# Optimization experiments

Measured on AMD Instinct MI355X. Metric: run time of the kernel, lower is better.

The kernel has to match this reference:

```python
import jax, jax.numpy as jnp
import numpy as np

NUM_EXPERTS = 8

def setup_inputs() -> dict:
    key = jax.random.key(0)
    k1, k2, k3, k4, k5 = jax.random.split(key, 5)
    T, D, H, O, E, K = 4096, 1024, 2048, 1024, NUM_EXPERTS, 2
    hidden_states = jax.random.normal(k1, (T, D), dtype=jnp.float32)
    top_k_indices = jax.random.randint(k2, (T, K), 0, E, dtype=jnp.int64)
    top_k_weights = jax.random.uniform(k3, (T, K), dtype=jnp.float32)
    gate_up_proj = jax.random.normal(k4, (E, 2 * H, D), dtype=jnp.float32) * 0.02
    down_proj = jax.random.normal(k5, (E, O, H), dtype=jnp.float32) * 0.02
    return {
        "hidden_states": hidden_states,
        "top_k_indices": top_k_indices,
        "top_k_weights": top_k_weights,
        "gate_up_proj": gate_up_proj,
        "down_proj": down_proj,
    }


def _moe(hidden_states, top_k_weights, gate_up_proj, down_proj, top_k_indices):
    # Mathematically identical to the torch per-token-gather loop, expressed as
    # dense all-expert compute + sparse combine (non-selected experts get weight 0).
    T = hidden_states.shape[0]
    E = gate_up_proj.shape[0]
    # [T, E, 2H]
    gate_up = jnp.einsum('td,ehd->teh', hidden_states, gate_up_proj)
    gate, up = jnp.split(gate_up, 2, axis=-1)
    h = jax.nn.silu(gate) * up  # [T, E, H]
    expert_out = jnp.einsum('teh,eoh->teo', h, down_proj)  # [T, E, O]
    # combine weights: scatter top-k routing weights into [T, E]
    combine = jnp.zeros((T, E), dtype=hidden_states.dtype)
    rows = jnp.arange(T)[:, None]
    combine = combine.at[rows, top_k_indices].add(top_k_weights)
    return jnp.einsum('teo,te->to', expert_out, combine)


def reference(hidden_states, top_k_indices, top_k_weights, gate_up_proj, down_proj):
    return _moe(hidden_states, top_k_weights, gate_up_proj, down_proj, top_k_indices)
```

## Files before the change

### kernel.cpp

```cpp
#include <hip/hip_runtime.h>
#include <stdint.h>

#define TOKS 4096
#define DIM  1024
#define HID  2048
#define OUTD 1024
#define NE   8
#define MP   9216
#define NBR  72

typedef __bf16 bf16;
typedef bf16 bf16x8 __attribute__((ext_vector_type(8)));
typedef float f32x4 __attribute__((ext_vector_type(4)));
typedef __attribute__((address_space(1))) void gvoid;
typedef __attribute__((address_space(3))) void lvoid;

#define WGU_OFF  0ull
#define WD_OFF   (WGU_OFF + 67108864ull)
#define XG_OFF   (WD_OFF  + 33554432ull)
#define H_OFF    (XG_OFF  + 18874368ull)
#define TK_OFF   (H_OFF   + 37748736ull)
#define META_OFF (TK_OFF  + 36864ull)
#define T2S_OFF  (META_OFF + 1024ull)
#define O0_OFF   WGU_OFF
#define O1_OFF   (WGU_OFF + 18874368ull)

__device__ __forceinline__ unsigned short f2bf(float f) {
  union { float f; unsigned u; } v; v.f = f;
  unsigned r = (v.u + 0x7FFFu + ((v.u >> 16) & 1u)) >> 16;
  return (unsigned short)r;
}
__device__ __forceinline__ float bf2f(unsigned short h) {
  union { unsigned u; float f; } v; v.u = ((unsigned)h) << 16; return v.f;
}
__device__ __forceinline__ unsigned pack2(float a, float b) {
  return (unsigned)f2bf(a) | ((unsigned)f2bf(b) << 16);
}
__device__ __forceinline__ void cp16(const void* g, void* l) {
  __builtin_amdgcn_global_load_lds((gvoid*)(void*)g, (lvoid*)l, 16, 0, 0);
}

#define CONVB_GU (NE * 2 * HID * DIM / 4 / 1024)
#define CONVB_X  (TOKS * DIM / 4 / 1024)
__global__ __launch_bounds__(1024) void route_conv_kernel(
    const int* __restrict__ idx, int* __restrict__ table,
    int* __restrict__ slot_token, int* __restrict__ tok2slot,
    const float4* __restrict__ srcGu, uint2* __restrict__ dstGu,
    const float4* __restrict__ srcX, uint2* __restrict__ dstXg) {
  if (blockIdx.x != 0) {
    int b = (int)blockIdx.x - 1;
    const float4* src; uint2* dst; int i;
    if (b < CONVB_GU) { i = b * 1024 + threadIdx.x; src = srcGu; dst = dstGu; }
    else              { i = (b - CONVB_GU) * 1024 + threadIdx.x; src = srcX; dst = dstXg; }
    float4 v = src[i];
    uint2 o; o.x = pack2(v.x, v.y); o.y = pack2(v.z, v.w);
    dst[i] = o;
    return;
  }
  __shared__ int cnt[NE], offs[NE], cur[NE];
  const int tid = threadIdx.x, lane = tid & 63;
  for (int i = tid; i < MP; i += 1024) slot_token[i] = -1;
  if (tid < NE) cnt[tid] = 0;
  __syncthreads();
  int myE[8];
#pragma unroll
  for (int c = 0; c < 8; ++c) myE[c] = idx[c * 1024 + tid];
#pragma unroll
  for (int c = 0; c < 8; ++c) {
    int e = myE[c];
#pragma unroll
    for (int ex = 0; ex < NE; ++ex) {
      unsigned long long m = __ballot(e == ex);
      if (lane == 0 && m) atomicAdd(&cnt[ex], __popcll(m));
    }
  }
  __syncthreads();
  if (tid == 0) {
    int cum = 0;
    for (int e = 0; e < NE; ++e) {
      offs[e] = cum; cur[e] = 0;
      int nb = (cnt[e] + 127) >> 7;
      int bb = cum >> 7;
      for (int b = 0; b < nb; ++b) table[bb + b] = e;
      cum += nb << 7;
    }
    for (int b = cum >> 7; b < NBR; ++b) table[b] = -1;
  }
  __syncthreads();
#pragma unroll
  for (int c = 0; c < 8; ++c) {
    int e = myE[c];
    int pos = 0;
#pragma unroll
    for (int ex = 0; ex < NE; ++ex) {
      unsigned long long m = __ballot(e == ex);
      if (e == ex) {
        int rank = __popcll(m & ((1ull << lane) - 1ull));
        int leader = __ffsll(m) - 1;
        int base = 0;
        if (lane == leader) base = atomicAdd(&cur[ex], __popcll(m));
        base = __shfl(base, leader);
        pos = offs[ex] + base + rank;
      }
    }
    slot_token[pos] = (c * 1024 + tid) >> 1;
    tok2slot[c * 1024 + tid] = pos;
  }
}

__global__ void combine_kernel(const unsigned short* __restrict__ O0,
                               const unsigned short* __restrict__ O1,
                               const int* __restrict__ tok2slot,
                               const float* __restrict__ wts, float4* __restrict__ out) {
  int t = blockIdx.x, c = threadIdx.x;
  int s0 = tok2slot[2 * t], s1 = tok2slot[2 * t + 1];
  float w0 = wts[2 * t], w1 = wts[2 * t + 1];
  uint2 a0 = ((const uint2*)(O0 + (size_t)s0 * OUTD))[c];
  uint2 b0 = ((const uint2*)(O1 + (size_t)s0 * OUTD))[c];
  uint2 a1 = ((const uint2*)(O0 + (size_t)s1 * OUTD))[c];
  uint2 b1 = ((const uint2*)(O1 + (size_t)s1 * OUTD))[c];
  float4 o;
  o.x = w0 * (bf2f(a0.x & 0xFFFF) + bf2f(b0.x & 0xFFFF)) + w1 * (bf2f(a1.x & 0xFFFF) + bf2f(b1.x & 0xFFFF));
  o.y = w0 * (bf2f(a0.x >> 16)    + bf2f(b0.x >> 16))    + w1 * (bf2f(a1.x >> 16)    + bf2f(b1.x >> 16));
  o.z = w0 * (bf2f(a0.y & 0xFFFF) + bf2f(b0.y & 0xFFFF)) + w1 * (bf2f(a1.y & 0xFFFF) + bf2f(b1.y & 0xFFFF));
  o.w = w0 * (bf2f(a0.y >> 16)    + bf2f(b0.y >> 16))    + w1 * (bf2f(a1.y >> 16)    + bf2f(b1.y >> 16));
  out[(size_t)t * (OUTD / 4) + c] = o;
}

#define WD_N4 (NE * OUTD * HID / 4)
#define CVT_NB 576
__global__ __launch_bounds__(256) void gemm1_kernel(
    const unsigned short* __restrict__ Xg,
    const unsigned short* __restrict__ Wgu,
    unsigned short* __restrict__ Hbuf,
    const int* __restrict__ table,
    const int* __restrict__ slot_token,
    const float4* __restrict__ srcD, uint2* __restrict__ dstD) {
  if (blockIdx.x >= 32) {
    const int cid = (blockIdx.x - 32) + 8 * blockIdx.y;
    const int NT = CVT_NB * 256;
    for (int i = cid * 256 + (int)threadIdx.x; i < WD_N4; i += NT) {
      float4 v = srcD[i];
      uint2 o; o.x = pack2(v.x, v.y); o.y = pack2(v.z, v.w);
      dstD[i] = o;
    }
    return;
  }
  int e = table[blockIdx.y];
  if (e < 0) return;
  const int tid = threadIdx.x;
  const int lane = tid & 63, wave = tid >> 6;
  const int wm = wave >> 1, wn = wave & 1;
  const int lr = lane & 15, quad = lane >> 4;

  __shared__ bf16 As[128 * 64];
  __shared__ bf16 Bg[64 * 64];
  __shared__ bf16 Bu[64 * 64];

  const int r0 = tid >> 3;
  size_t abase[4];
#pragma unroll
  for (int i = 0; i < 4; ++i) {
    int t = slot_token[blockIdx.y * 128 + i * 32 + r0];
    if (t < 0) t = 0;
    abase[i] = (size_t)t * DIM;
  }

  const unsigned short* Wg_base = Wgu + (size_t)e * 2 * HID * DIM + (size_t)(blockIdx.x * 64) * DIM;
  const unsigned short* Wu_base = Wg_base + (size_t)HID * DIM;

  f32x4 accg[4][2] = {}; f32x4 accu[4][2] = {};

  for (int kt = 0; kt < DIM / 64; ++kt) {
    const int kb = kt * 64;
#pragma unroll
    for (int i = 0; i < 4; ++i) {
      int s = i * 256 + tid, row = s >> 3, pc = s & 7, gc = pc ^ (row & 7);
      cp16(Xg + abase[i] + kb + gc * 8, (void*)(As + row * 64 + pc * 8));
    }
#pragma unroll
    for (int i = 0; i < 2; ++i) {
      int s = i * 256 + tid, row = s >> 3, pc = s & 7, gc = pc ^ (row & 7);
      cp16(Wg_base + (size_t)row * DIM + kb + gc * 8, (void*)(Bg + row * 64 + pc * 8));
      cp16(Wu_base + (size_t)row * DIM + kb + gc * 8, (void*)(Bu + row * 64 + pc * 8));
    }
    __syncthreads();
#pragma unroll
    for (int ks = 0; ks < 2; ++ks) {
      bf16x8 a[4], bg[2], bu[2];
#pragma unroll
      for (int i = 0; i < 4; ++i) {
        int row = wm * 64 + i * 16 + lr;
        int pc = (ks * 4 + quad) ^ (row & 7);
        a[i] = *(const bf16x8*)(As + row * 64 + pc * 8);
      }
#pragma unroll
      for (int j = 0; j < 2; ++j) {
        int row = wn * 32 + j * 16 + lr;
        int pc = (ks * 4 + quad) ^ (row & 7);
        bg[j] = *(const bf16x8*)(Bg + row * 64 + pc * 8);
        bu[j] = *(const bf16x8*)(Bu + row * 64 + pc * 8);
      }
#pragma unroll
      for (int i = 0; i < 4; ++i)
#pragma unroll
        for (int j = 0; j < 2; ++j) {
          accg[i][j] = __builtin_amdgcn_mfma_f32_16x16x32_bf16(a[i], bg[j], accg[i][j], 0, 0, 0);
          accu[i][j] = __builtin_amdgcn_mfma_f32_16x16x32_bf16(a[i], bu[j], accu[i][j], 0, 0, 0);
        }
    }
    __syncthreads();
  }

  const int rowBase = blockIdx.y * 128 + wm * 64;
  const int colBase = blockIdx.x * 64 + wn * 32;
#pragma unroll
  for (int i = 0; i < 4; ++i)
#pragma unroll
    for (int r = 0; r < 4; ++r) {
      int row = rowBase + i * 16 + quad * 4 + r;
#pragma unroll
      for (int j = 0; j < 2; ++j) {
        float g = accg[i][j][r], u = accu[i][j][r];
        float s = g / (1.0f + __expf(-g));
        Hbuf[(size_t)row * HID + colBase + j * 16 + lr] = f2bf(s * u);
      }
    }
}

__global__ __launch_bounds__(256) void gemm2_kernel(
    const unsigned short* __restrict__ Hbuf,
    const unsigned short* __restrict__ Wd,
    unsigned short* __restrict__ O0,
    unsigned short* __restrict__ O1,
    const int* __restrict__ table) {
  int e = table[blockIdx.y];
  if (e < 0) return;
  const int tid = threadIdx.x;
  const int lane = tid & 63, wave = tid >> 6;
  const int wm = wave >> 1, wn = wave & 1;
  const int lr = lane & 15, quad = lane >> 4;
  const int kslice = blockIdx.z;

  __shared__ bf16 As[128 * 64];
  __shared__ bf16 Bs[128 * 64];

  const unsigned short* A_base = Hbuf + (size_t)blockIdx.y * 128 * HID + kslice * (HID / 2);
  const unsigned short* B_base = Wd + (size_t)e * OUTD * HID + (size_t)(blockIdx.x * 128) * HID
                               + kslice * (HID / 2);

  f32x4 acc[4][4] = {};

  for (int kt = 0; kt < (HID / 2) / 64; ++kt) {
    const int kb = kt * 64;
#pragma unroll
    for (int i = 0; i < 4; ++i) {
      int s = i * 256 + tid, row = s >> 3, pc = s & 7, gc = pc ^ (row & 7);
      cp16(A_base + (size_t)row * HID + kb + gc * 8, (void*)(As + row * 64 + pc * 8));
      cp16(B_base + (size_t)row * HID + kb + gc * 8, (void*)(Bs + row * 64 + pc * 8));
    }
    __syncthreads();
#pragma unroll
    for (int ks = 0; ks < 2; ++ks) {
      bf16x8 a[4], b[4];
#pragma unroll
      for (int i = 0; i < 4; ++i) {
        int row = wm * 64 + i * 16 + lr;
        int pc = (ks * 4 + quad) ^ (row & 7);
        a[i] = *(const bf16x8*)(As + row * 64 + pc * 8);
      }
#pragma unroll
      for (int j = 0; j < 4; ++j) {
        int row = wn * 64 + j * 16 + lr;
        int pc = (ks * 4 + quad) ^ (row & 7);
        b[j] = *(const bf16x8*)(Bs + row * 64 + pc * 8);
      }
#pragma unroll
      for (int i = 0; i < 4; ++i)
#pragma unroll
        for (int j = 0; j < 4; ++j)
          acc[i][j] = __builtin_amdgcn_mfma_f32_16x16x32_bf16(a[i], b[j], acc[i][j], 0, 0, 0);
    }
    __syncthreads();
  }

  unsigned short* O = kslice ? O1 : O0;
  const int rowBase = blockIdx.y * 128 + wm * 64;
  const int colBase = blockIdx.x * 128 + wn * 64;
#pragma unroll
  for (int i = 0; i < 4; ++i)
#pragma unroll
    for (int r = 0; r < 4; ++r) {
      int row = rowBase + i * 16 + quad * 4 + r;
      unsigned short* Orow = O + (size_t)row * OUTD + colBase;
#pragma unroll
      for (int j = 0; j < 4; ++j)
        Orow[j * 16 + lr] = f2bf(acc[i][j][r]);
    }
}

extern "C" void kernel_launch(void* const* d_in, const int* in_sizes, int n_in,
                              void* d_out, int out_size, void* d_ws, size_t ws_size,
                              hipStream_t stream) {
  const float* X     = (const float*)d_in[0];
  const int*   idx   = (const int*)d_in[1];
  const float* wts   = (const float*)d_in[2];
  const float* WguF  = (const float*)d_in[3];
  const float* WdF   = (const float*)d_in[4];
  float* out = (float*)d_out;

  char* base = (char*)d_ws;
  unsigned short* Wgu = (unsigned short*)(base + WGU_OFF);
  unsigned short* Wd  = (unsigned short*)(base + WD_OFF);
  unsigned short* Xg  = (unsigned short*)(base + XG_OFF);
  unsigned short* Hb  = (unsigned short*)(base + H_OFF);
  unsigned short* O0  = (unsigned short*)(base + O0_OFF);
  unsigned short* O1  = (unsigned short*)(base + O1_OFF);
  int* slot_token = (int*)(base + TK_OFF);
  int* table      = (int*)(base + META_OFF);
  int* tok2slot   = (int*)(base + T2S_OFF);

  route_conv_kernel<<<1 + CONVB_GU + CONVB_X, 1024, 0, stream>>>(idx, table, slot_token, tok2slot,
      (const float4*)WguF, (uint2*)Wgu, (const float4*)X, (uint2*)Xg);
  gemm1_kernel<<<dim3(40, NBR), 256, 0, stream>>>(Xg, Wgu, Hb, table, slot_token,
      (const float4*)WdF, (uint2*)Wd);
  gemm2_kernel<<<dim3(OUTD / 128, NBR, 2), 256, 0, stream>>>(Hb, Wd, O0, O1, table);
  combine_kernel<<<TOKS, 256, 0, stream>>>(O0, O1, tok2slot, wts, (float4*)out);
}
```

Measured before the change: 398.6 us.

## Grid-stride weight conversion, split gemm1 launch, remap gemm2 blocks for L2 locality

The fp32-to-bf16 conversion now uses a fixed grid of 2560 blocks with a grid-stride loop, replacing one block per 1024 float4s. gemm1 is issued as two launches over halves of the row blocks, passing a ybase offset. gemm2 remaps its linear block id so that blocks which run at the same time share experts and weight tiles, aiming to improve L2 reuse across the XCD-interleaved dispatch. These changes add index arithmetic and one extra launch in exchange for better cache locality and less block-scheduling overhead.

```diff
diff --git a/kernel.cpp b/kernel.cpp
--- a/kernel.cpp
+++ b/kernel.cpp
@@ -40,8 +40,10 @@
   __builtin_amdgcn_global_load_lds((gvoid*)(void*)g, (lvoid*)l, 16, 0, 0);
 }
 
-#define CONVB_GU (NE * 2 * HID * DIM / 4 / 1024)
-#define CONVB_X  (TOKS * DIM / 4 / 1024)
+#define N4_GU (NE * 2 * HID * DIM / 4)
+#define N4_X  (TOKS * DIM / 4)
+#define N4_TOT (N4_GU + N4_X)
+#define NCONV 2560
 __global__ __launch_bounds__(1024) void route_conv_kernel(
     const int* __restrict__ idx, int* __restrict__ table,
     int* __restrict__ slot_token, int* __restrict__ tok2slot,
@@ -49,12 +51,13 @@
     const float4* __restrict__ srcX, uint2* __restrict__ dstXg) {
   if (blockIdx.x != 0) {
     int b = (int)blockIdx.x - 1;
-    const float4* src; uint2* dst; int i;
-    if (b < CONVB_GU) { i = b * 1024 + threadIdx.x; src = srcGu; dst = dstGu; }
-    else              { i = (b - CONVB_GU) * 1024 + threadIdx.x; src = srcX; dst = dstXg; }
-    float4 v = src[i];
-    uint2 o; o.x = pack2(v.x, v.y); o.y = pack2(v.z, v.w);
-    dst[i] = o;
+    for (int i = b * 1024 + (int)threadIdx.x; i < N4_TOT; i += NCONV * 1024) {
+      float4 v; uint2* dp;
+      if (i < N4_GU) { v = srcGu[i]; dp = dstGu + i; }
+      else           { v = srcX[i - N4_GU]; dp = dstXg + (i - N4_GU); }
+      uint2 o; o.x = pack2(v.x, v.y); o.y = pack2(v.z, v.w);
+      *dp = o;
+    }
     return;
   }
   __shared__ int cnt[NE], offs[NE], cur[NE];
@@ -135,9 +138,11 @@
     unsigned short* __restrict__ Hbuf,
     const int* __restrict__ table,
     const int* __restrict__ slot_token,
-    const float4* __restrict__ srcD, uint2* __restrict__ dstD) {
+    const float4* __restrict__ srcD, uint2* __restrict__ dstD,
+    int ybase) {
+  const int by = ybase + (int)blockIdx.y;
   if (blockIdx.x >= 32) {
-    const int cid = (blockIdx.x - 32) + 8 * blockIdx.y;
+    const int cid = ((int)blockIdx.x - 32) + 8 * by;
     const int NT = CVT_NB * 256;
     for (int i = cid * 256 + (int)threadIdx.x; i < WD_N4; i += NT) {
       float4 v = srcD[i];
@@ -146,7 +151,7 @@
     }
     return;
   }
-  int e = table[blockIdx.y];
+  int e = table[by];
   if (e < 0) return;
   const int tid = threadIdx.x;
   const int lane = tid & 63, wave = tid >> 6;
@@ -161,7 +166,7 @@
   size_t abase[4];
 #pragma unroll
   for (int i = 0; i < 4; ++i) {
-    int t = slot_token[blockIdx.y * 128 + i * 32 + r0];
+    int t = slot_token[by * 128 + i * 32 + r0];
     if (t < 0) t = 0;
     abase[i] = (size_t)t * DIM;
   }
@@ -212,7 +217,7 @@
     __syncthreads();
   }
 
-  const int rowBase = blockIdx.y * 128 + wm * 64;
+  const int rowBase = by * 128 + wm * 64;
   const int colBase = blockIdx.x * 64 + wn * 32;
 #pragma unroll
   for (int i = 0; i < 4; ++i)
@@ -234,19 +239,25 @@
     unsigned short* __restrict__ O0,
     unsigned short* __restrict__ O1,
     const int* __restrict__ table) {
-  int e = table[blockIdx.y];
+  const int h = (int)blockIdx.x + 8 * (int)blockIdx.y + 576 * (int)blockIdx.z;
+  const int c = h & 7, j = h >> 3;
+  const int wx = j & 7;
+  const int gi = c * 18 + (j >> 3);
+  const int wy = gi % 72, wz = gi / 72;
+
+  int e = table[wy];
   if (e < 0) return;
   const int tid = threadIdx.x;
   const int lane = tid & 63, wave = tid >> 6;
   const int wm = wave >> 1, wn = wave & 1;
   const int lr = lane & 15, quad = lane >> 4;
-  const int kslice = blockIdx.z;
+  const int kslice = wz;
 
   __shared__ bf16 As[128 * 64];
   __shared__ bf16 Bs[128 * 64];
 
-  const unsigned short* A_base = Hbuf + (size_t)blockIdx.y * 128 * HID + kslice * (HID / 2);
-  const unsigned short* B_base = Wd + (size_t)e * OUTD * HID + (size_t)(blockIdx.x * 128) * HID
+  const unsigned short* A_base = Hbuf + (size_t)wy * 128 * HID + kslice * (HID / 2);
+  const unsigned short* B_base = Wd + (size_t)e * OUTD * HID + (size_t)(wx * 128) * HID
                                + kslice * (HID / 2);
 
   f32x4 acc[4][4] = {};
@@ -270,23 +281,23 @@
         a[i] = *(const bf16x8*)(As + row * 64 + pc * 8);
       }
 #pragma unroll
-      for (int j = 0; j < 4; ++j) {
-        int row = wn * 64 + j * 16 + lr;
+      for (int j2 = 0; j2 < 4; ++j2) {
+        int row = wn * 64 + j2 * 16 + lr;
         int pc = (ks * 4 + quad) ^ (row & 7);
-        b[j] = *(const bf16x8*)(Bs + row * 64 + pc * 8);
+        b[j2] = *(const bf16x8*)(Bs + row * 64 + pc * 8);
       }
 #pragma unroll
       for (int i = 0; i < 4; ++i)
 #pragma unroll
-        for (int j = 0; j < 4; ++j)
-          acc[i][j] = __builtin_amdgcn_mfma_f32_16x16x32_bf16(a[i], b[j], acc[i][j], 0, 0, 0);
+        for (int j2 = 0; j2 < 4; ++j2)
+          acc[i][j2] = __builtin_amdgcn_mfma_f32_16x16x32_bf16(a[i], b[j2], acc[i][j2], 0, 0, 0);
     }
     __syncthreads();
   }
 
   unsigned short* O = kslice ? O1 : O0;
-  const int rowBase = blockIdx.y * 128 + wm * 64;
-  const int colBase = blockIdx.x * 128 + wn * 64;
+  const int rowBase = wy * 128 + wm * 64;
+  const int colBase = wx * 128 + wn * 64;
 #pragma unroll
   for (int i = 0; i < 4; ++i)
 #pragma unroll
@@ -294,8 +305,8 @@
       int row = rowBase + i * 16 + quad * 4 + r;
       unsigned short* Orow = O + (size_t)row * OUTD + colBase;
 #pragma unroll
-      for (int j = 0; j < 4; ++j)
-        Orow[j * 16 + lr] = f2bf(acc[i][j][r]);
+      for (int j2 = 0; j2 < 4; ++j2)
+        Orow[j2 * 16 + lr] = f2bf(acc[i][j2][r]);
     }
 }
 
@@ -320,10 +331,12 @@
   int* table      = (int*)(base + META_OFF);
   int* tok2slot   = (int*)(base + T2S_OFF);
 
-  route_conv_kernel<<<1 + CONVB_GU + CONVB_X, 1024, 0, stream>>>(idx, table, slot_token, tok2slot,
+  route_conv_kernel<<<1 + NCONV, 1024, 0, stream>>>(idx, table, slot_token, tok2slot,
       (const float4*)WguF, (uint2*)Wgu, (const float4*)X, (uint2*)Xg);
-  gemm1_kernel<<<dim3(40, NBR), 256, 0, stream>>>(Xg, Wgu, Hb, table, slot_token,
-      (const float4*)WdF, (uint2*)Wd);
-  gemm2_kernel<<<dim3(OUTD / 128, NBR, 2), 256, 0, stream>>>(Hb, Wd, O0, O1, table);
+  gemm1_kernel<<<dim3(40, 36), 256, 0, stream>>>(Xg, Wgu, Hb, table, slot_token,
+      (const float4*)WdF, (uint2*)Wd, 0);
+  gemm1_kernel<<<dim3(40, 36), 256, 0, stream>>>(Xg, Wgu, Hb, table, slot_token,
+      (const float4*)WdF, (uint2*)Wd, 36);
+  gemm2_kernel<<<dim3(8, NBR, 2), 256, 0, stream>>>(Hb, Wd, O0, O1, table);
   combine_kernel<<<TOKS, 256, 0, stream>>>(O0, O1, tok2slot, wts, (float4*)out);
 }
```

Measured after the change: 405.3 us. No clear change (+1.7%).

## Double-buffer LDS tiles with K=32 stages in both expert GEMMs

Applied to the files above, without the earlier changes.

Both grouped GEMM kernels now split K into 32-wide stages held in two LDS buffers. The async copy of the next stage is issued before the MFMAs on the current stage, so global loads overlap with compute instead of sitting behind a barrier. The swizzle is adapted to 32-element rows. Each stage does half as many MFMAs per barrier, and total LDS per block is unchanged.

```diff
diff --git a/kernel.cpp b/kernel.cpp
--- a/kernel.cpp
+++ b/kernel.cpp
@@ -137,7 +137,7 @@
     const int* __restrict__ slot_token,
     const float4* __restrict__ srcD, uint2* __restrict__ dstD) {
   if (blockIdx.x >= 32) {
-    const int cid = (blockIdx.x - 32) + 8 * blockIdx.y;
+    const int cid = ((int)blockIdx.x - 32) + 8 * (int)blockIdx.y;
     const int NT = CVT_NB * 256;
     for (int i = cid * 256 + (int)threadIdx.x; i < WD_N4; i += NT) {
       float4 v = srcD[i];
@@ -153,15 +153,15 @@
   const int wm = wave >> 1, wn = wave & 1;
   const int lr = lane & 15, quad = lane >> 4;
 
-  __shared__ bf16 As[128 * 64];
-  __shared__ bf16 Bg[64 * 64];
-  __shared__ bf16 Bu[64 * 64];
-
-  const int r0 = tid >> 3;
-  size_t abase[4];
-#pragma unroll
-  for (int i = 0; i < 4; ++i) {
-    int t = slot_token[blockIdx.y * 128 + i * 32 + r0];
+  __shared__ bf16 As[2][128 * 32];
+  __shared__ bf16 Bg[2][64 * 32];
+  __shared__ bf16 Bu[2][64 * 32];
+
+  const int r0 = tid >> 2;
+  size_t abase[2];
+#pragma unroll
+  for (int i = 0; i < 2; ++i) {
+    int t = slot_token[blockIdx.y * 128 + i * 64 + r0];
     if (t < 0) t = 0;
     abase[i] = (size_t)t * DIM;
   }
@@ -171,44 +171,53 @@
 
   f32x4 accg[4][2] = {}; f32x4 accu[4][2] = {};
 
-  for (int kt = 0; kt < DIM / 64; ++kt) {
-    const int kb = kt * 64;
+  auto stage = [&](bf16* as, bf16* bg, bf16* bu, int kt) {
+    const int kb = kt * 32;
+#pragma unroll
+    for (int i = 0; i < 2; ++i) {
+      int s = i * 256 + tid, row = s >> 2, p = s & 3, gc = p ^ ((row >> 1) & 3);
+      cp16(Xg + abase[i] + kb + gc * 8, (void*)(as + row * 32 + p * 8));
+    }
+    {
+      int s = tid, row = s >> 2, p = s & 3, gc = p ^ ((row >> 1) & 3);
+      cp16(Wg_base + (size_t)row * DIM + kb + gc * 8, (void*)(bg + row * 32 + p * 8));
+      cp16(Wu_base + (size_t)row * DIM + kb + gc * 8, (void*)(bu + row * 32 + p * 8));
+    }
+  };
+
+  auto compute = [&](const bf16* as, const bf16* bg, const bf16* bu) {
+    bf16x8 a[4], g[2], u[2];
 #pragma unroll
     for (int i = 0; i < 4; ++i) {
-      int s = i * 256 + tid, row = s >> 3, pc = s & 7, gc = pc ^ (row & 7);
-      cp16(Xg + abase[i] + kb + gc * 8, (void*)(As + row * 64 + pc * 8));
-    }
-#pragma unroll
-    for (int i = 0; i < 2; ++i) {
-      int s = i * 256 + tid, row = s >> 3, pc = s & 7, gc = pc ^ (row & 7);
-      cp16(Wg_base + (size_t)row * DIM + kb + gc * 8, (void*)(Bg + row * 64 + pc * 8));
-      cp16(Wu_base + (size_t)row * DIM + kb + gc * 8, (void*)(Bu + row * 64 + pc * 8));
-    }
+      int row = wm * 64 + i * 16 + lr;
+      int p = quad ^ ((row >> 1) & 3);
+      a[i] = *(const bf16x8*)(as + row * 32 + p * 8);
+    }
+#pragma unroll
+    for (int j = 0; j < 2; ++j) {
+      int row = wn * 32 + j * 16 + lr;
+      int p = quad ^ ((row >> 1) & 3);
+      g[j] = *(const bf16x8*)(bg + row * 32 + p * 8);
+      u[j] = *(const bf16x8*)(bu + row * 32 + p * 8);
+    }
+#pragma unroll
+    for (int i = 0; i < 4; ++i)
+#pragma unroll
+      for (int j = 0; j < 2; ++j) {
+        accg[i][j] = __builtin_amdgcn_mfma_f32_16x16x32_bf16(a[i], g[j], accg[i][j], 0, 0, 0);
+        accu[i][j] = __builtin_amdgcn_mfma_f32_16x16x32_bf16(a[i], u[j], accu[i][j], 0, 0, 0);
+      }
+  };
+
+  stage(As[0], Bg[0], Bu[0], 0);
+  __syncthreads();
+#pragma unroll 1
+  for (int kt = 0; kt < DIM / 32; kt += 2) {
+    stage(As[1], Bg[1], Bu[1], kt + 1);
+    compute(As[0], Bg[0], Bu[0]);
     __syncthreads();
-#pragma unroll
-    for (int ks = 0; ks < 2; ++ks) {
-      bf16x8 a[4], bg[2], bu[2];
-#pragma unroll
-      for (int i = 0; i < 4; ++i) {
-        int row = wm * 64 + i * 16 + lr;
-        int pc = (ks * 4 + quad) ^ (row & 7);
-        a[i] = *(const bf16x8*)(As + row * 64 + pc * 8);
-      }
-#pragma unroll
-      for (int j = 0; j < 2; ++j) {
-        int row = wn * 32 + j * 16 + lr;
-        int pc = (ks * 4 + quad) ^ (row & 7);
-        bg[j] = *(const bf16x8*)(Bg + row * 64 + pc * 8);
-        bu[j] = *(const bf16x8*)(Bu + row * 64 + pc * 8);
-      }
-#pragma unroll
-      for (int i = 0; i < 4; ++i)
-#pragma unroll
-        for (int j = 0; j < 2; ++j) {
-          accg[i][j] = __builtin_amdgcn_mfma_f32_16x16x32_bf16(a[i], bg[j], accg[i][j], 0, 0, 0);
-          accu[i][j] = __builtin_amdgcn_mfma_f32_16x16x32_bf16(a[i], bu[j], accu[i][j], 0, 0, 0);
-        }
-    }
+    if (kt + 2 < DIM / 32) stage(As[0], Bg[0], Bu[0], kt + 2);
+    compute(As[1], Bg[1], Bu[1]);
     __syncthreads();
   }
 
@@ -242,8 +251,8 @@
   const int lr = lane & 15, quad = lane >> 4;
   const int kslice = blockIdx.z;
 
-  __shared__ bf16 As[128 * 64];
-  __shared__ bf16 Bs[128 * 64];
+  __shared__ bf16 As[2][128 * 32];
+  __shared__ bf16 Bs[2][128 * 32];
 
   const unsigned short* A_base = Hbuf + (size_t)blockIdx.y * 128 * HID + kslice * (HID / 2);
   const unsigned short* B_base = Wd + (size_t)e * OUTD * HID + (size_t)(blockIdx.x * 128) * HID
@@ -251,36 +260,46 @@
 
   f32x4 acc[4][4] = {};
 
-  for (int kt = 0; kt < (HID / 2) / 64; ++kt) {
-    const int kb = kt * 64;
+  auto stage = [&](bf16* as, bf16* bs, int kt) {
+    const int kb = kt * 32;
+#pragma unroll
+    for (int i = 0; i < 2; ++i) {
+      int s = i * 256 + tid, row = s >> 2, p = s & 3, gc = p ^ ((row >> 1) & 3);
+      cp16(A_base + (size_t)row * HID + kb + gc * 8, (void*)(as + row * 32 + p * 8));
+      cp16(B_base + (size_t)row * HID + kb + gc * 8, (void*)(bs + row * 32 + p * 8));
+    }
+  };
+
+  auto compute = [&](const bf16* as, const bf16* bs) {
+    bf16x8 a[4], b[4];
 #pragma unroll
     for (int i = 0; i < 4; ++i) {
-      int s = i * 256 + tid, row = s >> 3, pc = s & 7, gc = pc ^ (row & 7);
-      cp16(A_base + (size_t)row * HID + kb + gc * 8, (void*)(As + row * 64 + pc * 8));
-      cp16(B_base + (size_t)row * HID + kb + gc * 8, (void*)(Bs + row * 64 + pc * 8));
-    }
+      int row = wm * 64 + i * 16 + lr;
+      int p = quad ^ ((row >> 1) & 3);
+      a[i] = *(const bf16x8*)(as + row * 32 + p * 8);
+    }
+#pragma unroll
+    for (int j = 0; j < 4; ++j) {
+      int row = wn * 64 + j * 16 + lr;
+      int p = quad ^ ((row >> 1) & 3);
+      b[j] = *(const bf16x8*)(bs + row * 32 + p * 8);
+    }
+#pragma unroll
+    for (int i = 0; i < 4; ++i)
+#pragma unroll
+      for (int j = 0; j < 4; ++j)
+        acc[i][j] = __builtin_amdgcn_mfma_f32_16x16x32_bf16(a[i], b[j], acc[i][j], 0, 0, 0);
+  };
+
+  stage(As[0], Bs[0], 0);
+  __syncthreads();
+#pragma unroll 1
+  for (int kt = 0; kt < (HID / 2) / 32; kt += 2) {
+    stage(As[1], Bs[1], kt + 1);
+    compute(As[0], Bs[0]);
     __syncthreads();
-#pragma unroll
-    for (int ks = 0; ks < 2; ++ks) {
-      bf16x8 a[4], b[4];
-#pragma unroll
-      for (int i = 0; i < 4; ++i) {
-        int row = wm * 64 + i * 16 + lr;
-        int pc = (ks * 4 + quad) ^ (row & 7);
-        a[i] = *(const bf16x8*)(As + row * 64 + pc * 8);
-      }
-#pragma unroll
-      for (int j = 0; j < 4; ++j) {
-        int row = wn * 64 + j * 16 + lr;
-        int pc = (ks * 4 + quad) ^ (row & 7);
-        b[j] = *(const bf16x8*)(Bs + row * 64 + pc * 8);
-      }
-#pragma unroll
-      for (int i = 0; i < 4; ++i)
-#pragma unroll
-        for (int j = 0; j < 4; ++j)
-          acc[i][j] = __builtin_amdgcn_mfma_f32_16x16x32_bf16(a[i], b[j], acc[i][j], 0, 0, 0);
-    }
+    if (kt + 2 < (HID / 2) / 32) stage(As[0], Bs[0], kt + 2);
+    compute(As[1], Bs[1]);
     __syncthreads();
   }
 
@@ -324,6 +343,6 @@
       (const float4*)WguF, (uint2*)Wgu, (const float4*)X, (uint2*)Xg);
   gemm1_kernel<<<dim3(40, NBR), 256, 0, stream>>>(Xg, Wgu, Hb, table, slot_token,
       (const float4*)WdF, (uint2*)Wd);
-  gemm2_kernel<<<dim3(OUTD / 128, NBR, 2), 256, 0, stream>>>(Hb, Wd, O0, O1, table);
+  gemm2_kernel<<<dim3(8, NBR, 2), 256, 0, stream>>>(Hb, Wd, O0, O1, table);
   combine_kernel<<<TOKS, 256, 0, stream>>>(O0, O1, tok2slot, wts, (float4*)out);
 }
```

After: 442.6 us. 11.0% more time.
